# Optimization experiments

Measured on AMD Instinct MI355X. Metric: run time of the kernel, lower is better.

Reference implementation:

```python
import jax, jax.numpy as jnp
import numpy as np

MU = 1.0
VUL = 1.0
M = 1.0
ETA = 0.5

BATCH = 256
NBIT = 64
NCLASS = 100
TRAIN_SIZE = 200000


def setup_inputs() -> dict:
    key = jax.random.key(0)
    k1, k2, k3, k4, k5 = jax.random.split(key, 5)
    u = jax.random.normal(k1, (BATCH, NBIT), dtype=jnp.float32)
    labels = jax.random.randint(k2, (BATCH,), 0, NCLASS)
    y = jax.nn.one_hot(labels, NCLASS, dtype=jnp.float32)
    # unique indices into the training-set buffers
    ind = jax.random.permutation(k3, TRAIN_SIZE)[:BATCH]
    U = jax.random.normal(k4, (NBIT, TRAIN_SIZE), dtype=jnp.float32)
    buf_labels = jax.random.randint(k5, (TRAIN_SIZE,), 0, NCLASS)
    Y = jax.nn.one_hot(buf_labels, NCLASS, dtype=jnp.float32).T  # (nclass, train_size)
    C = jnp.sign(jax.random.normal(jax.random.fold_in(key, 7), (NBIT, NCLASS), dtype=jnp.float32))
    return {"u": u, "y": y, "ind": ind, "U": U, "Y": Y, "C": C}


def _discrete_center(C, y, b):
    """Discrete cyclic coordinate descent over class rows. C: (nbit, nclass)."""
    Ct = C.T                      # (nclass, nbit)
    Yt = y.T                      # (nclass, batch)
    Q = Yt @ b.T                  # (nclass, nbit), constant across iterations
    G = Yt @ Yt.T                 # (nclass, nclass) Gram of label rows
    nclass = Ct.shape[0]

    def body(i, Ct):
        w = G[:, i].at[i].set(0.0)          # Y_prime @ v, self row excluded
        colsum = Ct.sum(axis=0) - Ct[i]     # C_prime.T @ ones
        new_row = jnp.sign(Q[i] - Ct.T @ w - VUL * colsum)
        return Ct.at[i].set(new_row)

    Ct = jax.lax.fori_loop(0, nclass, body, Ct)
    return Ct.T  # back to (nbit, nclass)


def reference(u, y, ind, U, Y, C):
    yf = y.astype(jnp.float32)
    # persistent buffer updates (detached in the original via .data)
    U_new = U.at[:, ind].set(jax.lax.stop_gradient(u.T))
    Y_new = Y.at[:, ind].set(yf.T)
    # binary targets for this batch
    b = jax.lax.stop_gradient(jnp.sign(MU * (C @ yf.T) + u.T))  # (nbit, batch)
    # DCC update of class centers (runs under no_grad in the original)
    C_new = _discrete_center(jax.lax.stop_gradient(C), jax.lax.stop_gradient(yf), b)
    # pairwise similarity loss against the whole training buffer
    s = (yf @ Y_new > 0).astype(u.dtype)                 # (batch, train_size)
    ip = jnp.clip(u @ U_new * 0.5, -100.0, 50.0)          # (batch, train_size)
    metric_loss = jnp.mean((1.0 - s) * jnp.log1p(jnp.exp(M + ip))
                           + s * jnp.log1p(jnp.exp(M - ip)))
    quantization_loss = jnp.mean((b - u.T) ** 2)
    loss = metric_loss + ETA * quantization_loss
    return loss, C_new
```

## Files before the change

kernel.cpp:

```cpp
#include <hip/hip_runtime.h>

#define T_TOTAL 200000
#define BATCH 256
#define NBIT 64
#define NCLASS 100
#define TN 128
#define NBLK ((T_TOTAL + TN - 1) / TN)

typedef __attribute__((ext_vector_type(8))) short bf16x8;
typedef __attribute__((ext_vector_type(4))) float f32x4;

#define LOG2E 1.4426950408889634f
#define LN2   0.6931471805599453

__device__ __forceinline__ unsigned short f2bf(float v) {
    union { float f; unsigned int u; } x; x.f = v;
    unsigned int r = x.u + 0x7fffu + ((x.u >> 16) & 1u);
    return (unsigned short)(r >> 16);
}

__device__ __forceinline__ float sgnf(float v) {
    return (v > 0.f) ? 1.f : ((v < 0.f) ? -1.f : 0.f);
}

__global__ __launch_bounds__(256) void prep_kernel(const float* __restrict__ y,
                                                   int* __restrict__ lab,
                                                   double* __restrict__ acc) {
    int idx = blockIdx.x * 256 + threadIdx.x;
    if (idx == 0) acc[0] = 0.0;
    if (idx < BATCH * NCLASS) {
        float v = y[idx];
        if (v > 0.5f) lab[idx / NCLASS] = idx % NCLASS;
    }
}

__global__ __launch_bounds__(256) void dcc_kernel(const float* __restrict__ u,
                                                  const float* __restrict__ C,
                                                  const int* __restrict__ lab,
                                                  float* __restrict__ out_c,
                                                  float* __restrict__ quant_out) {
    __shared__ float Q[NCLASS][NBIT];
    __shared__ float Ct[NCLASS][NBIT];
    __shared__ float wq[4];

    const int tid = threadIdx.x;
    const int k   = tid & 63;
    const int g   = tid >> 6;

    for (int o = tid; o < NCLASS * NBIT; o += 256) {
        ((float*)Q)[o] = 0.f;
        int i = o >> 6, kk = o & 63;
        Ct[i][kk] = C[kk * NCLASS + i];
    }
    __syncthreads();

    float qloc = 0.f;
    for (int jj = 0; jj < 64; ++jj) {
        int j = g * 64 + jj;
        int lj = lab[j];
        float uu = u[j * NBIT + k];
        float b = sgnf(C[k * NCLASS + lj] + uu);
        atomicAdd(&Q[lj][k], b);
        float d = b - uu;
        qloc += d * d;
    }
    for (int off = 32; off; off >>= 1) qloc += __shfl_xor(qloc, off);
    if ((tid & 63) == 0) wq[g] = qloc;
    __syncthreads();
    if (tid == 0) quant_out[0] = wq[0] + wq[1] + wq[2] + wq[3];

    if (tid < 64) {
        float total = 0.f;
        for (int i = 0; i < NCLASS; ++i) total += Ct[i][k];
        for (int i = 0; i < NCLASS; ++i) {
            float old = Ct[i][k];
            float v = Q[i][k] - (total - old);
            float nr = sgnf(v);
            Ct[i][k] = nr;
            total += nr - old;
        }
    }
    __syncthreads();
    for (int o = tid; o < NCLASS * NBIT; o += 256) {
        int kk = o / NCLASS, i = o - kk * NCLASS;
        out_c[o] = Ct[i][kk];
    }
}

__global__ __launch_bounds__(256) void metric_kernel(const float* __restrict__ u,
                                                     const float* __restrict__ U,
                                                     const float* __restrict__ Y,
                                                     const int* __restrict__ ind,
                                                     const int* __restrict__ lab,
                                                     double* __restrict__ acc) {
    __shared__ unsigned short Bt[TN][72];
    __shared__ int   labT[TN];
    __shared__ float labP[2][TN];
    __shared__ int   labB[BATCH];
    __shared__ float wpart[4];

    const int tid = threadIdx.x;
    const long t0 = (long)blockIdx.x * TN;

    labB[tid] = lab[tid];

    {
        const int c = tid & 127;
        const int h = tid >> 7;
        const long t = t0 + c;
        const bool ok = (t < (long)T_TOTAL);
        #pragma unroll
        for (int gg = 0; gg < 4; ++gg) {
            const int k0 = h * 32 + gg * 8;
            unsigned int w[4];
            #pragma unroll
            for (int p = 0; p < 4; ++p) {
                float v0 = 0.f, v1 = 0.f;
                if (ok) {
                    v0 = U[(long)(k0 + 2 * p) * T_TOTAL + t];
                    v1 = U[(long)(k0 + 2 * p + 1) * T_TOTAL + t];
                }
                w[p] = (unsigned int)f2bf(v0) | ((unsigned int)f2bf(v1) << 16);
            }
            uint4 q = make_uint4(w[0], w[1], w[2], w[3]);
            *reinterpret_cast<uint4*>(&Bt[c][k0]) = q;
        }
        float lp = 0.f;
        if (ok) {
            for (int r = 0; r < 50; ++r) {
                int row = h * 50 + r;
                lp = fmaf(Y[(long)row * T_TOTAL + t], (float)row, lp);
            }
        }
        labP[h][c] = lp;
    }
    __syncthreads();
    if (tid < TN) {
        long t = t0 + tid;
        labT[tid] = (t < (long)T_TOTAL) ? (int)(labP[0][tid] + labP[1][tid]) : -1;
    }
    __syncthreads();
    {
        long t = (long)ind[tid];
        long c = t - t0;
        if (c >= 0 && c < TN) {
            labT[c] = labB[tid];
            #pragma unroll
            for (int gg = 0; gg < 8; ++gg) {
                const int k0 = gg * 8;
                unsigned int w[4];
                #pragma unroll
                for (int p = 0; p < 4; ++p) {
                    float v0 = u[tid * NBIT + k0 + 2 * p];
                    float v1 = u[tid * NBIT + k0 + 2 * p + 1];
                    w[p] = (unsigned int)f2bf(v0) | ((unsigned int)f2bf(v1) << 16);
                }
                *reinterpret_cast<uint4*>(&Bt[c][k0]) = make_uint4(w[0], w[1], w[2], w[3]);
            }
        }
    }
    __syncthreads();

    const int wid  = tid >> 6;
    const int lane = tid & 63;
    const int lr   = lane & 15;
    const int lk   = (lane >> 4) * 8;

    bf16x8 afrag[4][2];
    #pragma unroll
    for (int mt = 0; mt < 4; ++mt) {
        #pragma unroll
        for (int kb = 0; kb < 2; ++kb) {
            const int j = wid * 64 + mt * 16 + lr;
            const float4* s4 = reinterpret_cast<const float4*>(u + j * NBIT + kb * 32 + lk);
            float4 va = s4[0], vb = s4[1];
            union { bf16x8 v; unsigned int w[4]; } pk;
            pk.w[0] = (unsigned int)f2bf(va.x) | ((unsigned int)f2bf(va.y) << 16);
            pk.w[1] = (unsigned int)f2bf(va.z) | ((unsigned int)f2bf(va.w) << 16);
            pk.w[2] = (unsigned int)f2bf(vb.x) | ((unsigned int)f2bf(vb.y) << 16);
            pk.w[3] = (unsigned int)f2bf(vb.z) | ((unsigned int)f2bf(vb.w) << 16);
            afrag[mt][kb] = pk.v;
        }
    }
    int labR[4][4];
    #pragma unroll
    for (int mt = 0; mt < 4; ++mt)
        #pragma unroll
        for (int e = 0; e < 4; ++e)
            labR[mt][e] = labB[wid * 64 + mt * 16 + (lane >> 4) * 4 + e];

    float sum2 = 0.f;
    for (int nt = 0; nt < 8; ++nt) {
        if (t0 + nt * 16 >= (long)T_TOTAL) break;
        const int col = nt * 16 + lr;
        union { bf16x8 v; uint4 q; } b0, b1;
        b0.q = *reinterpret_cast<const uint4*>(&Bt[col][lk]);
        b1.q = *reinterpret_cast<const uint4*>(&Bt[col][32 + lk]);
        const int labc = labT[col];
        #pragma unroll
        for (int mt = 0; mt < 4; ++mt) {
            f32x4 acc4 = {0.f, 0.f, 0.f, 0.f};
            acc4 = __builtin_amdgcn_mfma_f32_16x16x32_bf16(afrag[mt][0], b0.v, acc4, 0, 0, 0);
            acc4 = __builtin_amdgcn_mfma_f32_16x16x32_bf16(afrag[mt][1], b1.v, acc4, 0, 0, 0);
            #pragma unroll
            for (int e = 0; e < 4; ++e) {
                float ip = 0.5f * acc4[e];
                ip = fminf(fmaxf(ip, -100.f), 50.f);
                bool s = (labc == labR[mt][e]);
                float x = 1.f + (s ? -ip : ip);
                float e2 = exp2f(x * LOG2E);
                sum2 += log2f(1.f + e2);
            }
        }
    }
    for (int off = 32; off; off >>= 1) sum2 += __shfl_xor(sum2, off);
    if (lane == 0) wpart[wid] = sum2;
    __syncthreads();
    if (tid == 0) {
        double bs = (double)(wpart[0] + wpart[1] + wpart[2] + wpart[3]) * LN2;
        atomicAdd(acc, bs);
    }
}

__global__ void fin_kernel(const double* __restrict__ acc,
                           const float* __restrict__ quant,
                           float* __restrict__ out0) {
    out0[0] = (float)(acc[0] / ((double)BATCH * (double)T_TOTAL)
                      + 0.5 * ((double)quant[0] / (double)(BATCH * NBIT)));
}

extern "C" void kernel_launch(void* const* d_in, const int* in_sizes, int n_in,
                              void* d_out, int out_size, void* d_ws, size_t ws_size,
                              hipStream_t stream) {
    const float* u   = (const float*)d_in[0];
    const float* y   = (const float*)d_in[1];
    const int*   ind = (const int*)d_in[2];
    const float* U   = (const float*)d_in[3];
    const float* Y   = (const float*)d_in[4];
    const float* C   = (const float*)d_in[5];
    float* out = (float*)d_out;

    double* acc   = (double*)d_ws;
    float*  quant = (float*)((char*)d_ws + 8);
    int*    lab   = (int*)((char*)d_ws + 64);

    prep_kernel<<<(BATCH * NCLASS + 255) / 256, 256, 0, stream>>>(y, lab, acc);
    dcc_kernel<<<1, 256, 0, stream>>>(u, C, lab, out + 1, quant);
    metric_kernel<<<NBLK, 256, 0, stream>>>(u, U, Y, ind, lab, acc);
    fin_kernel<<<1, 1, 0, stream>>>(acc, quant, out);
}
```

Before: 262.6 us.

## Split label extraction into a vectorized pass, pre-pack u to bf16, swizzle LDS

```diff
diff --git a/kernel.cpp b/kernel.cpp
--- a/kernel.cpp
+++ b/kernel.cpp
@@ -1,4 +1,5 @@
 #include <hip/hip_runtime.h>
+#include <hip/hip_bf16.h>
 
 #define T_TOTAL 200000
 #define BATCH 256
@@ -13,24 +14,57 @@
 #define LOG2E 1.4426950408889634f
 #define LN2   0.6931471805599453
 
-__device__ __forceinline__ unsigned short f2bf(float v) {
-    union { float f; unsigned int u; } x; x.f = v;
-    unsigned int r = x.u + 0x7fffu + ((x.u >> 16) & 1u);
-    return (unsigned short)(r >> 16);
-}
-
 __device__ __forceinline__ float sgnf(float v) {
     return (v > 0.f) ? 1.f : ((v < 0.f) ? -1.f : 0.f);
 }
 
-__global__ __launch_bounds__(256) void prep_kernel(const float* __restrict__ y,
-                                                   int* __restrict__ lab,
-                                                   double* __restrict__ acc) {
-    int idx = blockIdx.x * 256 + threadIdx.x;
-    if (idx == 0) acc[0] = 0.0;
-    if (idx < BATCH * NCLASS) {
-        float v = y[idx];
-        if (v > 0.5f) lab[idx / NCLASS] = idx % NCLASS;
+__device__ __forceinline__ unsigned int pk2(float a, float b) {
+    union { __hip_bfloat162 h2; unsigned int ui; } cv;
+    cv.h2 = __float22bfloat162_rn(make_float2(a, b));
+    return cv.ui;
+}
+
+__global__ __launch_bounds__(256) void prep_kernel(const float* __restrict__ u,
+                                                   const float* __restrict__ y,
+                                                   int* __restrict__ labB,
+                                                   unsigned short* __restrict__ Abf) {
+    const int gt = blockIdx.x * 256 + threadIdx.x;
+    {
+        const int f = gt * 2;
+        const int row = f >> 4, p = f & 15;
+        const float4* up = reinterpret_cast<const float4*>(u);
+        float4 a = up[f], b = up[f + 1];
+        uint4 w = make_uint4(pk2(0.5f * a.x, 0.5f * a.y), pk2(0.5f * a.z, 0.5f * a.w),
+                             pk2(0.5f * b.x, 0.5f * b.y), pk2(0.5f * b.z, 0.5f * b.w));
+        *reinterpret_cast<uint4*>(&Abf[row * 64 + p * 4]) = w;
+    }
+    if (gt < BATCH) {
+        const float4* yp = reinterpret_cast<const float4*>(y + gt * NCLASS);
+        int l = 0;
+        #pragma unroll
+        for (int p = 0; p < 25; ++p) {
+            float4 v = yp[p];
+            if (v.x > 0.5f) l = p * 4;
+            if (v.y > 0.5f) l = p * 4 + 1;
+            if (v.z > 0.5f) l = p * 4 + 2;
+            if (v.w > 0.5f) l = p * 4 + 3;
+        }
+        labB[gt] = l;
+    }
+}
+
+__global__ __launch_bounds__(256) void laby_kernel(const float* __restrict__ Y,
+                                                   int* __restrict__ lab_buf) {
+    const unsigned stride = gridDim.x * 256;
+    const float4* Y4 = reinterpret_cast<const float4*>(Y);
+    for (unsigned q = blockIdx.x * 256 + threadIdx.x; q < 5000000u; q += stride) {
+        float4 v = Y4[q];
+        unsigned r = q / 50000u;
+        unsigned t = (q - r * 50000u) * 4u;
+        if (v.x > 0.5f) lab_buf[t]     = (int)r;
+        if (v.y > 0.5f) lab_buf[t + 1] = (int)r;
+        if (v.z > 0.5f) lab_buf[t + 2] = (int)r;
+        if (v.w > 0.5f) lab_buf[t + 3] = (int)r;
     }
 }
 
@@ -41,12 +75,14 @@
                                                   float* __restrict__ quant_out) {
     __shared__ float Q[NCLASS][NBIT];
     __shared__ float Ct[NCLASS][NBIT];
+    __shared__ int   labL[BATCH];
     __shared__ float wq[4];
 
     const int tid = threadIdx.x;
     const int k   = tid & 63;
     const int g   = tid >> 6;
 
+    labL[tid] = lab[tid];
     for (int o = tid; o < NCLASS * NBIT; o += 256) {
         ((float*)Q)[o] = 0.f;
         int i = o >> 6, kk = o & 63;
@@ -57,9 +93,9 @@
     float qloc = 0.f;
     for (int jj = 0; jj < 64; ++jj) {
         int j = g * 64 + jj;
-        int lj = lab[j];
+        int lj = labL[j];
         float uu = u[j * NBIT + k];
-        float b = sgnf(C[k * NCLASS + lj] + uu);
+        float b = sgnf(Ct[lj][k] + uu);
         atomicAdd(&Q[lj][k], b);
         float d = b - uu;
         qloc += d * d;
@@ -87,75 +123,67 @@
     }
 }
 
-__global__ __launch_bounds__(256) void metric_kernel(const float* __restrict__ u,
-                                                     const float* __restrict__ U,
-                                                     const float* __restrict__ Y,
-                                                     const int* __restrict__ ind,
-                                                     const int* __restrict__ lab,
-                                                     double* __restrict__ acc) {
-    __shared__ unsigned short Bt[TN][72];
+__global__ __launch_bounds__(256, 6) void metric_kernel(const float* __restrict__ u,
+                                                        const float* __restrict__ U,
+                                                        const int* __restrict__ ind,
+                                                        const int* __restrict__ labB_g,
+                                                        const int* __restrict__ lab_buf,
+                                                        const unsigned short* __restrict__ Abf,
+                                                        double* __restrict__ partial) {
+    __shared__ unsigned short Bt[TN * 64];
     __shared__ int   labT[TN];
-    __shared__ float labP[2][TN];
     __shared__ int   labB[BATCH];
     __shared__ float wpart[4];
 
     const int tid = threadIdx.x;
     const long t0 = (long)blockIdx.x * TN;
 
-    labB[tid] = lab[tid];
+    labB[tid] = labB_g[tid];
+    if (tid < TN) {
+        long t = t0 + tid;
+        labT[tid] = (t < (long)T_TOTAL) ? lab_buf[t] : -1;
+    }
 
     {
         const int c = tid & 127;
         const int h = tid >> 7;
         const long t = t0 + c;
         const bool ok = (t < (long)T_TOTAL);
-        #pragma unroll
-        for (int gg = 0; gg < 4; ++gg) {
-            const int k0 = h * 32 + gg * 8;
+        const int sw = (c & 7) << 3;
+        #pragma unroll
+        for (int m = 0; m < 4; ++m) {
             unsigned int w[4];
             #pragma unroll
-            for (int p = 0; p < 4; ++p) {
+            for (int pp = 0; pp < 4; ++pp) {
+                const int kk = h * 32 + m * 8 + 2 * pp;
                 float v0 = 0.f, v1 = 0.f;
                 if (ok) {
-                    v0 = U[(long)(k0 + 2 * p) * T_TOTAL + t];
-                    v1 = U[(long)(k0 + 2 * p + 1) * T_TOTAL + t];
+                    v0 = U[(long)kk * T_TOTAL + t];
+                    v1 = U[(long)(kk + 1) * T_TOTAL + t];
                 }
-                w[p] = (unsigned int)f2bf(v0) | ((unsigned int)f2bf(v1) << 16);
+                w[pp] = pk2(v0, v1);
             }
-            uint4 q = make_uint4(w[0], w[1], w[2], w[3]);
-            *reinterpret_cast<uint4*>(&Bt[c][k0]) = q;
-        }
-        float lp = 0.f;
-        if (ok) {
-            for (int r = 0; r < 50; ++r) {
-                int row = h * 50 + r;
-                lp = fmaf(Y[(long)row * T_TOTAL + t], (float)row, lp);
-            }
-        }
-        labP[h][c] = lp;
-    }
-    __syncthreads();
-    if (tid < TN) {
-        long t = t0 + tid;
-        labT[tid] = (t < (long)T_TOTAL) ? (int)(labP[0][tid] + labP[1][tid]) : -1;
+            const int k0 = h * 32 + m * 8;
+            *reinterpret_cast<uint4*>(&Bt[c * 64 + (k0 ^ sw)]) = make_uint4(w[0], w[1], w[2], w[3]);
+        }
     }
     __syncthreads();
     {
-        long t = (long)ind[tid];
-        long c = t - t0;
+        long c = (long)ind[tid] - t0;
         if (c >= 0 && c < TN) {
             labT[c] = labB[tid];
+            const int ci = (int)c;
+            const int sw = (ci & 7) << 3;
             #pragma unroll
-            for (int gg = 0; gg < 8; ++gg) {
-                const int k0 = gg * 8;
+            for (int m = 0; m < 8; ++m) {
                 unsigned int w[4];
                 #pragma unroll
-                for (int p = 0; p < 4; ++p) {
-                    float v0 = u[tid * NBIT + k0 + 2 * p];
-                    float v1 = u[tid * NBIT + k0 + 2 * p + 1];
-                    w[p] = (unsigned int)f2bf(v0) | ((unsigned int)f2bf(v1) << 16);
+                for (int pp = 0; pp < 4; ++pp) {
+                    float v0 = u[tid * NBIT + m * 8 + 2 * pp];
+                    float v1 = u[tid * NBIT + m * 8 + 2 * pp + 1];
+                    w[pp] = pk2(v0, v1);
                 }
-                *reinterpret_cast<uint4*>(&Bt[c][k0]) = make_uint4(w[0], w[1], w[2], w[3]);
+                *reinterpret_cast<uint4*>(&Bt[ci * 64 + ((m * 8) ^ sw)]) = make_uint4(w[0], w[1], w[2], w[3]);
             }
         }
     }
@@ -164,7 +192,7 @@
     const int wid  = tid >> 6;
     const int lane = tid & 63;
     const int lr   = lane & 15;
-    const int lk   = (lane >> 4) * 8;
+    const int g4   = lane >> 4;
 
     bf16x8 afrag[4][2];
     #pragma unroll
@@ -172,13 +200,8 @@
         #pragma unroll
         for (int kb = 0; kb < 2; ++kb) {
             const int j = wid * 64 + mt * 16 + lr;
-            const float4* s4 = reinterpret_cast<const float4*>(u + j * NBIT + kb * 32 + lk);
-            float4 va = s4[0], vb = s4[1];
-            union { bf16x8 v; unsigned int w[4]; } pk;
-            pk.w[0] = (unsigned int)f2bf(va.x) | ((unsigned int)f2bf(va.y) << 16);
-            pk.w[1] = (unsigned int)f2bf(va.z) | ((unsigned int)f2bf(va.w) << 16);
-            pk.w[2] = (unsigned int)f2bf(vb.x) | ((unsigned int)f2bf(vb.y) << 16);
-            pk.w[3] = (unsigned int)f2bf(vb.z) | ((unsigned int)f2bf(vb.w) << 16);
+            union { bf16x8 v; uint4 q; } pk;
+            pk.q = *reinterpret_cast<const uint4*>(&Abf[j * 64 + kb * 32 + g4 * 8]);
             afrag[mt][kb] = pk.v;
         }
     }
@@ -187,15 +210,16 @@
     for (int mt = 0; mt < 4; ++mt)
         #pragma unroll
         for (int e = 0; e < 4; ++e)
-            labR[mt][e] = labB[wid * 64 + mt * 16 + (lane >> 4) * 4 + e];
+            labR[mt][e] = labB[wid * 64 + mt * 16 + g4 * 4 + e];
 
     float sum2 = 0.f;
     for (int nt = 0; nt < 8; ++nt) {
         if (t0 + nt * 16 >= (long)T_TOTAL) break;
         const int col = nt * 16 + lr;
+        const int sw = (col & 7) << 3;
         union { bf16x8 v; uint4 q; } b0, b1;
-        b0.q = *reinterpret_cast<const uint4*>(&Bt[col][lk]);
-        b1.q = *reinterpret_cast<const uint4*>(&Bt[col][32 + lk]);
+        b0.q = *reinterpret_cast<const uint4*>(&Bt[col * 64 + ((g4 * 8) ^ sw)]);
+        b1.q = *reinterpret_cast<const uint4*>(&Bt[col * 64 + ((32 + g4 * 8) ^ sw)]);
         const int labc = labT[col];
         #pragma unroll
         for (int mt = 0; mt < 4; ++mt) {
@@ -204,11 +228,10 @@
             acc4 = __builtin_amdgcn_mfma_f32_16x16x32_bf16(afrag[mt][1], b1.v, acc4, 0, 0, 0);
             #pragma unroll
             for (int e = 0; e < 4; ++e) {
-                float ip = 0.5f * acc4[e];
-                ip = fminf(fmaxf(ip, -100.f), 50.f);
-                bool s = (labc == labR[mt][e]);
-                float x = 1.f + (s ? -ip : ip);
-                float e2 = exp2f(x * LOG2E);
+                float ip = fminf(fmaxf(acc4[e], -100.f), 50.f);
+                float z  = (labc == labR[mt][e]) ? -ip : ip;
+                float tt = fmaf(z, LOG2E, LOG2E);
+                float e2 = exp2f(tt);
                 sum2 += log2f(1.f + e2);
             }
         }
@@ -216,17 +239,24 @@
     for (int off = 32; off; off >>= 1) sum2 += __shfl_xor(sum2, off);
     if (lane == 0) wpart[wid] = sum2;
     __syncthreads();
-    if (tid == 0) {
-        double bs = (double)(wpart[0] + wpart[1] + wpart[2] + wpart[3]) * LN2;
-        atomicAdd(acc, bs);
-    }
-}
-
-__global__ void fin_kernel(const double* __restrict__ acc,
-                           const float* __restrict__ quant,
-                           float* __restrict__ out0) {
-    out0[0] = (float)(acc[0] / ((double)BATCH * (double)T_TOTAL)
-                      + 0.5 * ((double)quant[0] / (double)(BATCH * NBIT)));
+    if (tid == 0)
+        partial[blockIdx.x] = (double)(wpart[0] + wpart[1] + wpart[2] + wpart[3]) * LN2;
+}
+
+__global__ __launch_bounds__(256) void fin_kernel(const double* __restrict__ partial,
+                                                  const float* __restrict__ quant,
+                                                  float* __restrict__ out0) {
+    __shared__ double wp[4];
+    double s = 0.0;
+    for (int i = threadIdx.x; i < NBLK; i += 256) s += partial[i];
+    for (int off = 32; off; off >>= 1) s += __shfl_xor(s, off);
+    if ((threadIdx.x & 63) == 0) wp[threadIdx.x >> 6] = s;
+    __syncthreads();
+    if (threadIdx.x == 0) {
+        double tot = wp[0] + wp[1] + wp[2] + wp[3];
+        out0[0] = (float)(tot / ((double)BATCH * (double)T_TOTAL)
+                          + 0.5 * ((double)quant[0] / (double)(BATCH * NBIT)));
+    }
 }
 
 extern "C" void kernel_launch(void* const* d_in, const int* in_sizes, int n_in,
@@ -240,12 +270,15 @@
     const float* C   = (const float*)d_in[5];
     float* out = (float*)d_out;
 
-    double* acc   = (double*)d_ws;
-    float*  quant = (float*)((char*)d_ws + 8);
-    int*    lab   = (int*)((char*)d_ws + 64);
-
-    prep_kernel<<<(BATCH * NCLASS + 255) / 256, 256, 0, stream>>>(y, lab, acc);
-    dcc_kernel<<<1, 256, 0, stream>>>(u, C, lab, out + 1, quant);
-    metric_kernel<<<NBLK, 256, 0, stream>>>(u, U, Y, ind, lab, acc);
-    fin_kernel<<<1, 1, 0, stream>>>(acc, quant, out);
-}
+    float*          quant   = (float*)d_ws;
+    int*            labB    = (int*)((char*)d_ws + 64);
+    unsigned short* Abf     = (unsigned short*)((char*)d_ws + 2048);
+    double*         partial = (double*)((char*)d_ws + 36864);
+    int*            lab_buf = (int*)((char*)d_ws + 65536);
+
+    prep_kernel<<<8, 256, 0, stream>>>(u, y, labB, Abf);
+    laby_kernel<<<2048, 256, 0, stream>>>(Y, lab_buf);
+    dcc_kernel<<<1, 256, 0, stream>>>(u, C, labB, out + 1, quant);
+    metric_kernel<<<NBLK, 256, 0, stream>>>(u, U, ind, labB, lab_buf, Abf, partial);
+    fin_kernel<<<1, 256, 0, stream>>>(partial, quant, out);
+}
```

Result: slower. 277.6 us (+5.7%).
